# Kernel tuning notes

Measured on AMD Instinct MI355X. Metric: run time of the kernel, lower is better.

Reference implementation:

```python
import jax, jax.numpy as jnp
import numpy as np

NEG_SLOPE = 0.2  # PyG GATv2Conv default negative_slope


def gatv2_conv(x, src, dst, Wl, bl, Wr, br, att, bias, concat=True):
    # x: [N, Fin]; src/dst: [E] (message flows src -> dst, softmax over dst)
    N = x.shape[0]
    H, C = att.shape
    xl = (x @ Wl + bl).reshape(N, H, C)  # source-side transform (lin_l)
    xr = (x @ Wr + br).reshape(N, H, C)  # target-side transform (lin_r)
    e = xl[src] + xr[dst]                              # [E, H, C]
    score = jnp.sum(jax.nn.leaky_relu(e, NEG_SLOPE) * att, axis=-1)  # [E, H]
    # segment softmax over incoming edges of each target node
    m = jax.ops.segment_max(score, dst, num_segments=N)               # [N, H]
    a = jnp.exp(score - m[dst])
    denom = jax.ops.segment_sum(a, dst, num_segments=N)               # [N, H]
    alpha = a / denom[dst]                                            # [E, H]
    out = jax.ops.segment_sum(xl[src] * alpha[..., None], dst, num_segments=N)  # [N, H, C]
    if concat:
        out = out.reshape(N, H * C)
    else:
        out = out.mean(axis=1)
    return out + bias


def setup_inputs() -> dict:
    key = jax.random.key(0)
    ks = jax.random.split(key, 12)
    N, E, Fin = 100000, 1600000, 128
    H1, C1 = 8, 16
    C2 = 64
    def glorot(k, shape):
        fan_in, fan_out = shape[0], shape[-1]
        lim = (6.0 / (fan_in + fan_out)) ** 0.5
        return jax.random.uniform(k, shape, jnp.float32, -lim, lim)
    x = jax.random.normal(ks[0], (N, Fin), jnp.float32)
    edge_index = jax.random.randint(ks[1], (2, E), 0, N, dtype=jnp.int64)
    return {
        "x": x,
        "edge_index": edge_index,
        "Wl1": glorot(ks[2], (Fin, H1 * C1)),
        "bl1": jnp.zeros((H1 * C1,), jnp.float32),
        "Wr1": glorot(ks[3], (Fin, H1 * C1)),
        "br1": jnp.zeros((H1 * C1,), jnp.float32),
        "att1": glorot(ks[4], (H1, C1)),
        "bias1": jnp.zeros((H1 * C1,), jnp.float32),
        "Wl2": glorot(ks[5], (H1 * C1, C2)),
        "bl2": jnp.zeros((C2,), jnp.float32),
        "Wr2": glorot(ks[6], (H1 * C1, C2)),
        "br2": jnp.zeros((C2,), jnp.float32),
        "att2": glorot(ks[7], (1, C2)),
        "bias2": jnp.zeros((C2,), jnp.float32),
    }


def reference(x, edge_index, Wl1, bl1, Wr1, br1, att1, bias1,
              Wl2, bl2, Wr2, br2, att2, bias2):
    N = x.shape[0]
    loops = jnp.arange(N, dtype=edge_index.dtype)
    src = jnp.concatenate([edge_index[0], loops])  # PyG adds self loops by default
    dst = jnp.concatenate([edge_index[1], loops])
    # eval mode: F.dropout(training=False) is identity
    h = gatv2_conv(x, src, dst, Wl1, bl1, Wr1, br1, att1, bias1, concat=True)
    h = jax.nn.elu(h)
    out = gatv2_conv(h, src, dst, Wl2, bl2, Wr2, br2, att2, bias2, concat=True)
    return out
```

## Files before the change

kernel.cpp:

```cpp
#include <hip/hip_runtime.h>
#include <math.h>

#define FIN 128
#define F1  128
#define C2  64
#define NEG 0.2f

#define BKT_SHIFT 8
#define BKT_SIZE  256
#define SCAT_CHUNK 8192
#define IMGCAP 8192

typedef _Float16 half4 __attribute__((ext_vector_type(4)));
typedef _Float16 f16x8 __attribute__((ext_vector_type(8)));
typedef _Float16 h2    __attribute__((ext_vector_type(2)));
typedef float    f32x4 __attribute__((ext_vector_type(4)));

union H8u { f16x8 v; h2 p[4]; };

__global__ __launch_bounds__(256) void bucket_hist_kernel(
    const int* __restrict__ ei, int* __restrict__ bcnt, int E, int ET, int NBKT) {
  __shared__ int sh[512];
  const int t = threadIdx.x;
  for (int b = t; b < NBKT; b += 256) sh[b] = 0;
  __syncthreads();
  const int g0 = blockIdx.x * SCAT_CHUNK + t;
#pragma unroll
  for (int i = 0; i < 32; ++i) {
    const int g = g0 + i * 256;
    if (g < ET) {
      const int dst = (g < E) ? ei[E + g] : (g - E);
      atomicAdd(&sh[dst >> BKT_SHIFT], 1);
    }
  }
  __syncthreads();
  for (int b = t; b < NBKT; b += 256)
    if (sh[b]) atomicAdd(&bcnt[b], sh[b]);
}

__global__ __launch_bounds__(512) void bucket_scan_kernel(
    const int* __restrict__ bcnt, int* __restrict__ bbase, int* __restrict__ bcur,
    int* __restrict__ indptr, int NBKT, int N, int ET) {
  __shared__ int sh[512];
  const int t = threadIdx.x;
  const int v = (t < NBKT) ? bcnt[t] : 0;
  sh[t] = v;
  __syncthreads();
  for (int off = 1; off < 512; off <<= 1) {
    int val = (t >= off) ? sh[t - off] : 0;
    __syncthreads();
    sh[t] += val;
    __syncthreads();
  }
  const int excl = sh[t] - v;
  if (t < NBKT) { bbase[t] = excl; bcur[t] = excl; }
  if (t == NBKT - 1) bbase[NBKT] = excl + v;
  if (t == 0) indptr[N] = ET;
}

__global__ __launch_bounds__(256) void bucket_scatter_kernel(
    const int* __restrict__ ei, int* __restrict__ bcur, int* __restrict__ tmp,
    int E, int ET, int NBKT) {
  __shared__ int sh_hist[512];
  __shared__ int sh_base[512];
  const int t = threadIdx.x;
  for (int b = t; b < NBKT; b += 256) sh_hist[b] = 0;
  __syncthreads();
  const int g0 = blockIdx.x * SCAT_CHUNK + t;
  int bk[32], pk[32];
#pragma unroll
  for (int i = 0; i < 32; ++i) {
    const int g = g0 + i * 256;
    int b = -1, p = 0;
    if (g < ET) {
      const int src = (g < E) ? ei[g] : (g - E);
      const int dst = (g < E) ? ei[E + g] : (g - E);
      b = dst >> BKT_SHIFT;
      p = (src << BKT_SHIFT) | (dst & (BKT_SIZE - 1));
      atomicAdd(&sh_hist[b], 1);
    }
    bk[i] = b; pk[i] = p;
  }
  __syncthreads();
  for (int b = t; b < NBKT; b += 256) {
    const int c = sh_hist[b];
    sh_base[b] = c ? atomicAdd(&bcur[b], c) : 0;
    sh_hist[b] = 0;
  }
  __syncthreads();
#pragma unroll
  for (int i = 0; i < 32; ++i) {
    if (bk[i] >= 0) {
      const int off = atomicAdd(&sh_hist[bk[i]], 1);
      tmp[sh_base[bk[i]] + off] = pk[i];
    }
  }
}

__global__ __launch_bounds__(256) void build_csr_kernel(
    const int* __restrict__ tmp, const int* __restrict__ bbase,
    int* __restrict__ indptr, int* __restrict__ csr, int N) {
  __shared__ int cnt[256];
  __shared__ int cur[256];
  __shared__ int img[IMGCAP];
  const int b = blockIdx.x;
  const int t = threadIdx.x;
  const int base = bbase[b];
  const int cntb = bbase[b + 1] - base;
  cnt[t] = 0;
  __syncthreads();
  for (int i = t; i < cntb; i += 256)
    atomicAdd(&cnt[tmp[base + i] & (BKT_SIZE - 1)], 1);
  __syncthreads();
  const int v = cnt[t];
  cur[t] = v;
  __syncthreads();
  for (int off = 1; off < 256; off <<= 1) {
    int val = (t >= off) ? cur[t - off] : 0;
    __syncthreads();
    cur[t] += val;
    __syncthreads();
  }
  const int excl = cur[t] - v;
  const int node = (b << BKT_SHIFT) + t;
  if (node < N) indptr[node] = base + excl;
  __syncthreads();
  cur[t] = excl;
  __syncthreads();
  if (cntb <= IMGCAP) {
    for (int i = t; i < cntb; i += 256) {
      const int p = tmp[base + i];
      const int pos = atomicAdd(&cur[p & (BKT_SIZE - 1)], 1);
      img[pos] = p >> BKT_SHIFT;
    }
    __syncthreads();
    for (int i = t; i < cntb; i += 256) csr[base + i] = img[i];
  } else {
    for (int i = t; i < cntb; i += 256) {
      const int p = tmp[base + i];
      const int pos = atomicAdd(&cur[p & (BKT_SIZE - 1)], 1);
      csr[base + pos] = p >> BKT_SHIFT;
    }
  }
}

__global__ __launch_bounds__(256) void wtrans_kernel(
    const float* __restrict__ W0, const float* __restrict__ W1,
    const float* __restrict__ W2, const float* __restrict__ W3,
    _Float16* __restrict__ T0, _Float16* __restrict__ T1,
    _Float16* __restrict__ T2, _Float16* __restrict__ T3) {
  const int m = blockIdx.y;
  const float* W = (m == 0) ? W0 : (m == 1) ? W1 : (m == 2) ? W2 : W3;
  _Float16* T = (m == 0) ? T0 : (m == 1) ? T1 : (m == 2) ? T2 : T3;
  const int ncols = (m < 2) ? 128 : 64;
  const int idx = blockIdx.x * 256 + threadIdx.x;
  if (idx < ncols * 128) {
    const int n = idx >> 7;
    const int k = idx & 127;
    T[idx] = (_Float16)W[k * ncols + n];
  }
}

template<int NCOLS, int CPW, bool AF32>
__global__ __launch_bounds__(256) void gemm_dual_kernel(
    const void* __restrict__ Av,
    const _Float16* __restrict__ WtL, const float* __restrict__ bLp, _Float16* __restrict__ OL,
    const _Float16* __restrict__ WtR, const float* __restrict__ bRp, _Float16* __restrict__ ORp,
    int M) {
  const int wave = threadIdx.x >> 6;
  const int lane = threadIdx.x & 63;
  const int row16 = lane & 15;
  const int quad  = lane >> 4;
  const int kb = quad * 8;
  f16x8 bfL[CPW][4], bfR[CPW][4];
  float bvL[CPW], bvR[CPW];
#pragma unroll
  for (int c = 0; c < CPW; ++c) {
    const int n0 = (wave * CPW + c) * 16;
    bvL[c] = bLp[n0 + row16];
    bvR[c] = bRp[n0 + row16];
#pragma unroll
    for (int kt = 0; kt < 4; ++kt) {
      bfL[c][kt] = *(const f16x8*)(WtL + (n0 + row16) * 128 + kt * 32 + kb);
      bfR[c][kt] = *(const f16x8*)(WtR + (n0 + row16) * 128 + kt * 32 + kb);
    }
  }
  const int rowTiles = (M + 15) >> 4;
  for (int rt = blockIdx.x; rt < rowTiles; rt += gridDim.x) {
    const int r0 = rt << 4;
    const int arow = min(r0 + row16, M - 1);
    f16x8 af[4];
    if constexpr (AF32) {
      const float4* ap = (const float4*)Av + (size_t)arow * 32;
#pragma unroll
      for (int kt = 0; kt < 4; ++kt) {
        const float4 u = ap[kt * 8 + quad * 2];
        const float4 w = ap[kt * 8 + quad * 2 + 1];
        f16x8 h;
        h[0] = (_Float16)u.x; h[1] = (_Float16)u.y;
        h[2] = (_Float16)u.z; h[3] = (_Float16)u.w;
        h[4] = (_Float16)w.x; h[5] = (_Float16)w.y;
        h[6] = (_Float16)w.z; h[7] = (_Float16)w.w;
        af[kt] = h;
      }
    } else {
      const _Float16* A = (const _Float16*)Av;
#pragma unroll
      for (int kt = 0; kt < 4; ++kt)
        af[kt] = *(const f16x8*)(A + (size_t)arow * 128 + kt * 32 + kb);
    }
    f32x4 accL[CPW], accR[CPW];
#pragma unroll
    for (int c = 0; c < CPW; ++c) {
      accL[c] = (f32x4){0.f, 0.f, 0.f, 0.f};
      accR[c] = (f32x4){0.f, 0.f, 0.f, 0.f};
    }
#pragma unroll
    for (int kt = 0; kt < 4; ++kt) {
#pragma unroll
      for (int c = 0; c < CPW; ++c) {
        accL[c] = __builtin_amdgcn_mfma_f32_16x16x32_f16(af[kt], bfL[c][kt], accL[c], 0, 0, 0);
        accR[c] = __builtin_amdgcn_mfma_f32_16x16x32_f16(af[kt], bfR[c][kt], accR[c], 0, 0, 0);
      }
    }
#pragma unroll
    for (int c = 0; c < CPW; ++c) {
      const int col = (wave * CPW + c) * 16 + row16;
#pragma unroll
      for (int r = 0; r < 4; ++r) {
        const int row = r0 + quad * 4 + r;
        if (row < M) {
          OL[(size_t)row * NCOLS + col]  = (_Float16)(accL[c][r] + bvL[c]);
          ORp[(size_t)row * NCOLS + col] = (_Float16)(accR[c][r] + bvR[c]);
        }
      }
    }
  }
}

template<int LSH>
__device__ __forceinline__ void attn_load4(const _Float16* __restrict__ xlp,
                                           const int* __restrict__ csr,
                                           int e, int endm1,
                                           H8u& x0, H8u& x1, H8u& x2, H8u& x3) {
  const int s0 = csr[min(e,     endm1)];
  const int s1 = csr[min(e + 1, endm1)];
  const int s2 = csr[min(e + 2, endm1)];
  const int s3 = csr[min(e + 3, endm1)];
  x0.v = *(const f16x8*)(xlp + ((size_t)s0 << LSH));
  x1.v = *(const f16x8*)(xlp + ((size_t)s1 << LSH));
  x2.v = *(const f16x8*)(xlp + ((size_t)s2 << LSH));
  x3.v = *(const f16x8*)(xlp + ((size_t)s3 << LSH));
}

template<int XORS>
__device__ __forceinline__ void attn_batch(const H8u& x0, const H8u& x1,
                                           const H8u& x2, const H8u& x3,
                                           const H8u& xru, const H8u& atu,
                                           int rem, float& l, float (&acc)[8]) {
  const h2 neg2 = {(_Float16)NEG, (_Float16)NEG};
  const h2 zero2 = {(_Float16)0.f, (_Float16)0.f};
  h2 sa0 = zero2, sa1 = zero2, sa2 = zero2, sa3 = zero2;
#pragma unroll
  for (int j = 0; j < 4; ++j) {
    h2 e0 = x0.p[j] + xru.p[j];
    h2 e1 = x1.p[j] + xru.p[j];
    h2 e2 = x2.p[j] + xru.p[j];
    h2 e3 = x3.p[j] + xru.p[j];
    e0 = __builtin_elementwise_max(e0, e0 * neg2);
    e1 = __builtin_elementwise_max(e1, e1 * neg2);
    e2 = __builtin_elementwise_max(e2, e2 * neg2);
    e3 = __builtin_elementwise_max(e3, e3 * neg2);
    sa0 = e0 * atu.p[j] + sa0;
    sa1 = e1 * atu.p[j] + sa1;
    sa2 = e2 * atu.p[j] + sa2;
    sa3 = e3 * atu.p[j] + sa3;
  }
  float t0 = (float)sa0[0] + (float)sa0[1];
  float t1 = (float)sa1[0] + (float)sa1[1];
  float t2 = (float)sa2[0] + (float)sa2[1];
  float t3 = (float)sa3[0] + (float)sa3[1];
  t0 += __shfl_xor(t0, 1);  t1 += __shfl_xor(t1, 1);
  t2 += __shfl_xor(t2, 1);  t3 += __shfl_xor(t3, 1);
  if constexpr (XORS >= 2) {
    t0 += __shfl_xor(t0, 2);  t1 += __shfl_xor(t1, 2);
    t2 += __shfl_xor(t2, 2);  t3 += __shfl_xor(t3, 2);
  }
  if constexpr (XORS >= 3) {
    t0 += __shfl_xor(t0, 4);  t1 += __shfl_xor(t1, 4);
    t2 += __shfl_xor(t2, 4);  t3 += __shfl_xor(t3, 4);
  }
  const float p0 = __expf(t0);
  const float p1 = (rem > 1) ? __expf(t1) : 0.f;
  const float p2 = (rem > 2) ? __expf(t2) : 0.f;
  const float p3 = (rem > 3) ? __expf(t3) : 0.f;
  l += (p0 + p1) + (p2 + p3);
#pragma unroll
  for (int j = 0; j < 4; ++j) {
    acc[2*j]   = fmaf(p0, (float)x0.p[j][0], acc[2*j]);
    acc[2*j+1] = fmaf(p0, (float)x0.p[j][1], acc[2*j+1]);
    acc[2*j]   = fmaf(p1, (float)x1.p[j][0], acc[2*j]);
    acc[2*j+1] = fmaf(p1, (float)x1.p[j][1], acc[2*j+1]);
    acc[2*j]   = fmaf(p2, (float)x2.p[j][0], acc[2*j]);
    acc[2*j+1] = fmaf(p2, (float)x2.p[j][1], acc[2*j+1]);
    acc[2*j]   = fmaf(p3, (float)x3.p[j][0], acc[2*j]);
    acc[2*j+1] = fmaf(p3, (float)x3.p[j][1], acc[2*j+1]);
  }
}

__global__ __launch_bounds__(256) void attn1_kernel(
    const _Float16* __restrict__ xl, const _Float16* __restrict__ xr,
    const float* __restrict__ att, const float* __restrict__ bias,
    const int* __restrict__ indptr, const int* __restrict__ csr,
    _Float16* __restrict__ hout, int N) {
  const int lane = threadIdx.x & 15;
  const int v = blockIdx.x * 16 + (threadIdx.x >> 4);
  if (v >= N) return;
  const int c8 = lane << 3;
  const _Float16* xlp = xl + c8;
  H8u xru; xru.v = *(const f16x8*)(xr + ((size_t)v << 7) + c8);
  H8u atu;
  {
    const float4 a0 = *(const float4*)(att + c8);
    const float4 a1 = *(const float4*)(att + c8 + 4);
    f16x8 a;
    a[0] = (_Float16)a0.x; a[1] = (_Float16)a0.y; a[2] = (_Float16)a0.z; a[3] = (_Float16)a0.w;
    a[4] = (_Float16)a1.x; a[5] = (_Float16)a1.y; a[6] = (_Float16)a1.z; a[7] = (_Float16)a1.w;
    atu.v = a;
  }
  const int beg = indptr[v];
  const int end = indptr[v + 1];
  const int endm1 = end - 1;
  float l = 0.f;
  float acc[8] = {0.f, 0.f, 0.f, 0.f, 0.f, 0.f, 0.f, 0.f};

  H8u a0, a1, a2, a3, b0, b1, b2, b3;
  int e = beg;
  attn_load4<7>(xlp, csr, e, endm1, a0, a1, a2, a3);
  while (e + 4 < end) {
    attn_load4<7>(xlp, csr, e + 4, endm1, b0, b1, b2, b3);
    attn_batch<1>(a0, a1, a2, a3, xru, atu, 4, l, acc);
    e += 4;
    if (e + 4 < end) {
      attn_load4<7>(xlp, csr, e + 4, endm1, a0, a1, a2, a3);
      attn_batch<1>(b0, b1, b2, b3, xru, atu, 4, l, acc);
      e += 4;
    } else {
      const int rem = end - e;
      attn_batch<1>(b0, b1, b2, b3, xru, atu, rem, l, acc);
      e = end;
      break;
    }
  }
  if (e < end) attn_batch<1>(a0, a1, a2, a3, xru, atu, end - e, l, acc);

  const float rl = 1.f / l;
  const float4 bb0 = *(const float4*)(bias + c8);
  const float4 bb1 = *(const float4*)(bias + c8 + 4);
  float r[8];
  r[0] = fmaf(acc[0], rl, bb0.x); r[1] = fmaf(acc[1], rl, bb0.y);
  r[2] = fmaf(acc[2], rl, bb0.z); r[3] = fmaf(acc[3], rl, bb0.w);
  r[4] = fmaf(acc[4], rl, bb1.x); r[5] = fmaf(acc[5], rl, bb1.y);
  r[6] = fmaf(acc[6], rl, bb1.z); r[7] = fmaf(acc[7], rl, bb1.w);
  f16x8 hres;
#pragma unroll
  for (int i = 0; i < 8; ++i) {
    const float z = r[i] > 0.f ? r[i] : expm1f(r[i]);
    hres[i] = (_Float16)z;
  }
  *(f16x8*)(hout + ((size_t)v << 7) + c8) = hres;
}

__global__ __launch_bounds__(256) void attn2_kernel(
    const _Float16* __restrict__ xl, const _Float16* __restrict__ xr,
    const float* __restrict__ att, const float* __restrict__ bias,
    const int* __restrict__ indptr, const int* __restrict__ csr,
    float* __restrict__ out, int N) {
  const int lane = threadIdx.x & 7;
  const int v = blockIdx.x * 32 + (threadIdx.x >> 3);
  if (v >= N) return;
  const int c8 = lane << 3;
  const _Float16* xlp = xl + c8;
  H8u xru; xru.v = *(const f16x8*)(xr + ((size_t)v << 6) + c8);
  H8u atu;
  {
    const float4 a0 = *(const float4*)(att + c8);
    const float4 a1 = *(const float4*)(att + c8 + 4);
    f16x8 a;
    a[0] = (_Float16)a0.x; a[1] = (_Float16)a0.y; a[2] = (_Float16)a0.z; a[3] = (_Float16)a0.w;
    a[4] = (_Float16)a1.x; a[5] = (_Float16)a1.y; a[6] = (_Float16)a1.z; a[7] = (_Float16)a1.w;
    atu.v = a;
  }
  const int beg = indptr[v];
  const int end = indptr[v + 1];
  const int endm1 = end - 1;
  float l = 0.f;
  float acc[8] = {0.f, 0.f, 0.f, 0.f, 0.f, 0.f, 0.f, 0.f};

  H8u a0, a1, a2, a3, b0, b1, b2, b3;
  int e = beg;
  attn_load4<6>(xlp, csr, e, endm1, a0, a1, a2, a3);
  while (e + 4 < end) {
    attn_load4<6>(xlp, csr, e + 4, endm1, b0, b1, b2, b3);
    attn_batch<3>(a0, a1, a2, a3, xru, atu, 4, l, acc);
    e += 4;
    if (e + 4 < end) {
      attn_load4<6>(xlp, csr, e + 4, endm1, a0, a1, a2, a3);
      attn_batch<3>(b0, b1, b2, b3, xru, atu, 4, l, acc);
      e += 4;
    } else {
      const int rem = end - e;
      attn_batch<3>(b0, b1, b2, b3, xru, atu, rem, l, acc);
      e = end;
      break;
    }
  }
  if (e < end) attn_batch<3>(a0, a1, a2, a3, xru, atu, end - e, l, acc);

  const float rl = 1.f / l;
  const float4 bb0 = *(const float4*)(bias + c8);
  const float4 bb1 = *(const float4*)(bias + c8 + 4);
  float4 o0, o1;
  o0.x = fmaf(acc[0], rl, bb0.x); o0.y = fmaf(acc[1], rl, bb0.y);
  o0.z = fmaf(acc[2], rl, bb0.z); o0.w = fmaf(acc[3], rl, bb0.w);
  o1.x = fmaf(acc[4], rl, bb1.x); o1.y = fmaf(acc[5], rl, bb1.y);
  o1.z = fmaf(acc[6], rl, bb1.z); o1.w = fmaf(acc[7], rl, bb1.w);
  *(float4*)(out + ((size_t)v << 6) + c8) = o0;
  *(float4*)(out + ((size_t)v << 6) + c8 + 4) = o1;
}

extern "C" void kernel_launch(void* const* d_in, const int* in_sizes, int n_in,
                              void* d_out, int out_size, void* d_ws, size_t ws_size,
                              hipStream_t stream) {
  const float* x     = (const float*)d_in[0];
  const int*   ei    = (const int*)d_in[1];
  const float* Wl1   = (const float*)d_in[2];
  const float* bl1   = (const float*)d_in[3];
  const float* Wr1   = (const float*)d_in[4];
  const float* br1   = (const float*)d_in[5];
  const float* att1  = (const float*)d_in[6];
  const float* bias1 = (const float*)d_in[7];
  const float* Wl2   = (const float*)d_in[8];
  const float* bl2   = (const float*)d_in[9];
  const float* Wr2   = (const float*)d_in[10];
  const float* br2   = (const float*)d_in[11];
  const float* att2  = (const float*)d_in[12];
  const float* bias2 = (const float*)d_in[13];

  const int N  = in_sizes[0] / FIN;
  const int E  = in_sizes[1] / 2;
  const int ET = E + N;
  const int NBKT = (N + BKT_SIZE - 1) >> BKT_SHIFT;

  _Float16* xl1h  = (_Float16*)d_ws;
  _Float16* xr1h  = xl1h + (size_t)N * F1;
  _Float16* hbufh = xr1h + (size_t)N * F1;
  _Float16* Wt1l  = hbufh + (size_t)N * F1;
  _Float16* Wt1r  = Wt1l + 128 * 128;
  _Float16* Wt2l  = Wt1r + 128 * 128;
  _Float16* Wt2r  = Wt2l + 64 * 128;
  int* indptr = (int*)(Wt2r + 64 * 128);
  int* csr    = indptr + (N + 1);
  int* bcnt   = csr + ET;
  int* bbase  = bcnt + 512;
  int* bcur   = bbase + 513;
  int* tmp    = (int*)hbufh;
  _Float16* xl2h = xl1h;
  _Float16* xr2h = xr1h;
  float* out  = (float*)d_out;

  const int sblocks = (ET + SCAT_CHUNK - 1) / SCAT_CHUNK;

  hipMemsetAsync(bcnt, 0, 512 * sizeof(int), stream);
  bucket_hist_kernel<<<sblocks, 256, 0, stream>>>(ei, bcnt, E, ET, NBKT);
  bucket_scan_kernel<<<1, 512, 0, stream>>>(bcnt, bbase, bcur, indptr, NBKT, N, ET);
  bucket_scatter_kernel<<<sblocks, 256, 0, stream>>>(ei, bcur, tmp, E, ET, NBKT);
  build_csr_kernel<<<NBKT, 256, 0, stream>>>(tmp, bbase, indptr, csr, N);

  wtrans_kernel<<<dim3(64, 4), 256, 0, stream>>>(Wl1, Wr1, Wl2, Wr2, Wt1l, Wt1r, Wt2l, Wt2r);

  gemm_dual_kernel<128, 2, true><<<1024, 256, 0, stream>>>(
      x, Wt1l, bl1, xl1h, Wt1r, br1, xr1h, N);

  attn1_kernel<<<(N + 15) / 16, 256, 0, stream>>>(xl1h, xr1h, att1, bias1, indptr, csr, hbufh, N);

  gemm_dual_kernel<64, 1, false><<<1024, 256, 0, stream>>>(
      hbufh, Wt2l, bl2, xl2h, Wt2r, br2, xr2h, N);

  attn2_kernel<<<(N + 31) / 32, 256, 0, stream>>>(xl2h, xr2h, att2, bias2, indptr, csr, out, N);
}
```

Baseline: 348.4 us.

## Restructure attention edge loop into exact-size 8/4/2/1 blocks with fdot2 scoring

```diff
diff --git a/kernel.cpp b/kernel.cpp
--- a/kernel.cpp
+++ b/kernel.cpp
@@ -17,6 +17,16 @@
 typedef float    f32x4 __attribute__((ext_vector_type(4)));
 
 union H8u { f16x8 v; h2 p[4]; };
+
+#if __has_builtin(__builtin_amdgcn_fdot2)
+__device__ __forceinline__ float fdot2_acc(h2 a, h2 b, float c) {
+  return __builtin_amdgcn_fdot2(a, b, c, false);
+}
+#else
+__device__ __forceinline__ float fdot2_acc(h2 a, h2 b, float c) {
+  return c + (float)a[0] * (float)b[0] + (float)a[1] * (float)b[1];
+}
+#endif
 
 __global__ __launch_bounds__(256) void bucket_hist_kernel(
     const int* __restrict__ ei, int* __restrict__ bcnt, int E, int ET, int NBKT) {
@@ -238,74 +248,60 @@
   }
 }
 
-template<int LSH>
-__device__ __forceinline__ void attn_load4(const _Float16* __restrict__ xlp,
+template<int LSH, int XORS, int B>
+__device__ __forceinline__ void attn_block(const _Float16* __restrict__ xlp,
+                                           const int* __restrict__ csr, int e,
+                                           const H8u& xru, const H8u& atu,
+                                           float& l, float (&acc)[8]) {
+  const h2 neg2 = {(_Float16)NEG, (_Float16)NEG};
+  int s[B];
+#pragma unroll
+  for (int i = 0; i < B; ++i) s[i] = csr[e + i];
+  H8u x[B];
+#pragma unroll
+  for (int i = 0; i < B; ++i) x[i].v = *(const f16x8*)(xlp + ((size_t)s[i] << LSH));
+  float t[B];
+#pragma unroll
+  for (int i = 0; i < B; ++i) {
+    float tv = 0.f;
+#pragma unroll
+    for (int j = 0; j < 4; ++j) {
+      h2 ev = x[i].p[j] + xru.p[j];
+      ev = __builtin_elementwise_max(ev, ev * neg2);
+      tv = fdot2_acc(ev, atu.p[j], tv);
+    }
+    t[i] = tv;
+  }
+#pragma unroll
+  for (int i = 0; i < B; ++i) {
+    t[i] += __shfl_xor(t[i], 1);
+    if constexpr (XORS >= 2) t[i] += __shfl_xor(t[i], 2);
+    if constexpr (XORS >= 3) t[i] += __shfl_xor(t[i], 4);
+  }
+  float p[B];
+#pragma unroll
+  for (int i = 0; i < B; ++i) { p[i] = __expf(t[i]); l += p[i]; }
+#pragma unroll
+  for (int i = 0; i < B; ++i) {
+#pragma unroll
+    for (int j = 0; j < 4; ++j) {
+      acc[2*j]   = fmaf(p[i], (float)x[i].p[j][0], acc[2*j]);
+      acc[2*j+1] = fmaf(p[i], (float)x[i].p[j][1], acc[2*j+1]);
+    }
+  }
+}
+
+template<int LSH, int XORS>
+__device__ __forceinline__ void attn_edges(const _Float16* __restrict__ xlp,
                                            const int* __restrict__ csr,
-                                           int e, int endm1,
-                                           H8u& x0, H8u& x1, H8u& x2, H8u& x3) {
-  const int s0 = csr[min(e,     endm1)];
-  const int s1 = csr[min(e + 1, endm1)];
-  const int s2 = csr[min(e + 2, endm1)];
-  const int s3 = csr[min(e + 3, endm1)];
-  x0.v = *(const f16x8*)(xlp + ((size_t)s0 << LSH));
-  x1.v = *(const f16x8*)(xlp + ((size_t)s1 << LSH));
-  x2.v = *(const f16x8*)(xlp + ((size_t)s2 << LSH));
-  x3.v = *(const f16x8*)(xlp + ((size_t)s3 << LSH));
-}
-
-template<int XORS>
-__device__ __forceinline__ void attn_batch(const H8u& x0, const H8u& x1,
-                                           const H8u& x2, const H8u& x3,
+                                           int beg, int end,
                                            const H8u& xru, const H8u& atu,
-                                           int rem, float& l, float (&acc)[8]) {
-  const h2 neg2 = {(_Float16)NEG, (_Float16)NEG};
-  const h2 zero2 = {(_Float16)0.f, (_Float16)0.f};
-  h2 sa0 = zero2, sa1 = zero2, sa2 = zero2, sa3 = zero2;
-#pragma unroll
-  for (int j = 0; j < 4; ++j) {
-    h2 e0 = x0.p[j] + xru.p[j];
-    h2 e1 = x1.p[j] + xru.p[j];
-    h2 e2 = x2.p[j] + xru.p[j];
-    h2 e3 = x3.p[j] + xru.p[j];
-    e0 = __builtin_elementwise_max(e0, e0 * neg2);
-    e1 = __builtin_elementwise_max(e1, e1 * neg2);
-    e2 = __builtin_elementwise_max(e2, e2 * neg2);
-    e3 = __builtin_elementwise_max(e3, e3 * neg2);
-    sa0 = e0 * atu.p[j] + sa0;
-    sa1 = e1 * atu.p[j] + sa1;
-    sa2 = e2 * atu.p[j] + sa2;
-    sa3 = e3 * atu.p[j] + sa3;
-  }
-  float t0 = (float)sa0[0] + (float)sa0[1];
-  float t1 = (float)sa1[0] + (float)sa1[1];
-  float t2 = (float)sa2[0] + (float)sa2[1];
-  float t3 = (float)sa3[0] + (float)sa3[1];
-  t0 += __shfl_xor(t0, 1);  t1 += __shfl_xor(t1, 1);
-  t2 += __shfl_xor(t2, 1);  t3 += __shfl_xor(t3, 1);
-  if constexpr (XORS >= 2) {
-    t0 += __shfl_xor(t0, 2);  t1 += __shfl_xor(t1, 2);
-    t2 += __shfl_xor(t2, 2);  t3 += __shfl_xor(t3, 2);
-  }
-  if constexpr (XORS >= 3) {
-    t0 += __shfl_xor(t0, 4);  t1 += __shfl_xor(t1, 4);
-    t2 += __shfl_xor(t2, 4);  t3 += __shfl_xor(t3, 4);
-  }
-  const float p0 = __expf(t0);
-  const float p1 = (rem > 1) ? __expf(t1) : 0.f;
-  const float p2 = (rem > 2) ? __expf(t2) : 0.f;
-  const float p3 = (rem > 3) ? __expf(t3) : 0.f;
-  l += (p0 + p1) + (p2 + p3);
-#pragma unroll
-  for (int j = 0; j < 4; ++j) {
-    acc[2*j]   = fmaf(p0, (float)x0.p[j][0], acc[2*j]);
-    acc[2*j+1] = fmaf(p0, (float)x0.p[j][1], acc[2*j+1]);
-    acc[2*j]   = fmaf(p1, (float)x1.p[j][0], acc[2*j]);
-    acc[2*j+1] = fmaf(p1, (float)x1.p[j][1], acc[2*j+1]);
-    acc[2*j]   = fmaf(p2, (float)x2.p[j][0], acc[2*j]);
-    acc[2*j+1] = fmaf(p2, (float)x2.p[j][1], acc[2*j+1]);
-    acc[2*j]   = fmaf(p3, (float)x3.p[j][0], acc[2*j]);
-    acc[2*j+1] = fmaf(p3, (float)x3.p[j][1], acc[2*j+1]);
-  }
+                                           float& l, float (&acc)[8]) {
+  int e = beg;
+  for (; e + 8 <= end; e += 8) attn_block<LSH, XORS, 8>(xlp, csr, e, xru, atu, l, acc);
+  if (e + 4 <= end) { attn_block<LSH, XORS, 4>(xlp, csr, e, xru, atu, l, acc); e += 4; }
+  if (e + 2 <= end) { attn_block<LSH, XORS, 2>(xlp, csr, e, xru, atu, l, acc); e += 2; }
+  if (e < end)      { attn_block<LSH, XORS, 1>(xlp, csr, e, xru, atu, l, acc); }
 }
 
 __global__ __launch_bounds__(256) void attn1_kernel(
@@ -330,29 +326,9 @@
   }
   const int beg = indptr[v];
   const int end = indptr[v + 1];
-  const int endm1 = end - 1;
   float l = 0.f;
   float acc[8] = {0.f, 0.f, 0.f, 0.f, 0.f, 0.f, 0.f, 0.f};
-
-  H8u a0, a1, a2, a3, b0, b1, b2, b3;
-  int e = beg;
-  attn_load4<7>(xlp, csr, e, endm1, a0, a1, a2, a3);
-  while (e + 4 < end) {
-    attn_load4<7>(xlp, csr, e + 4, endm1, b0, b1, b2, b3);
-    attn_batch<1>(a0, a1, a2, a3, xru, atu, 4, l, acc);
-    e += 4;
-    if (e + 4 < end) {
-      attn_load4<7>(xlp, csr, e + 4, endm1, a0, a1, a2, a3);
-      attn_batch<1>(b0, b1, b2, b3, xru, atu, 4, l, acc);
-      e += 4;
-    } else {
-      const int rem = end - e;
-      attn_batch<1>(b0, b1, b2, b3, xru, atu, rem, l, acc);
-      e = end;
-      break;
-    }
-  }
-  if (e < end) attn_batch<1>(a0, a1, a2, a3, xru, atu, end - e, l, acc);
+  attn_edges<7, 1>(xlp, csr, beg, end, xru, atu, l, acc);
 
   const float rl = 1.f / l;
   const float4 bb0 = *(const float4*)(bias + c8);
@@ -393,29 +369,9 @@
   }
   const int beg = indptr[v];
   const int end = indptr[v + 1];
-  const int endm1 = end - 1;
   float l = 0.f;
   float acc[8] = {0.f, 0.f, 0.f, 0.f, 0.f, 0.f, 0.f, 0.f};
-
-  H8u a0, a1, a2, a3, b0, b1, b2, b3;
-  int e = beg;
-  attn_load4<6>(xlp, csr, e, endm1, a0, a1, a2, a3);
-  while (e + 4 < end) {
-    attn_load4<6>(xlp, csr, e + 4, endm1, b0, b1, b2, b3);
-    attn_batch<3>(a0, a1, a2, a3, xru, atu, 4, l, acc);
-    e += 4;
-    if (e + 4 < end) {
-      attn_load4<6>(xlp, csr, e + 4, endm1, a0, a1, a2, a3);
-      attn_batch<3>(b0, b1, b2, b3, xru, atu, 4, l, acc);
-      e += 4;
-    } else {
-      const int rem = end - e;
-      attn_batch<3>(b0, b1, b2, b3, xru, atu, rem, l, acc);
-      e = end;
-      break;
-    }
-  }
-  if (e < end) attn_batch<3>(a0, a1, a2, a3, xru, atu, end - e, l, acc);
+  attn_edges<6, 3>(xlp, csr, beg, end, xru, atu, l, acc);
 
   const float rl = 1.f / l;
   const float4 bb0 = *(const float4*)(bias + c8);
```

Result: no change. 342.6 us (-1.6%).
